# Kernel tuning notes

Measured on AMD Instinct MI355X. Metric: run time of the kernel, lower is better.

Reference implementation:

```python
import jax, jax.numpy as jnp
import numpy as np

B, W, KD, NC, D, NN, NH, AD, HOPS = 512, 4, 64, 32, 256, 16, 8, 32, 4
DH = D // NH
DFF = 4 * D
P = B * W + B
ROLE_WRITER, ROLE_QUERY = 0, 1


def setup_inputs() -> dict:
    key = jax.random.key(0)
    ks = iter(jax.random.split(key, 40))
    f = lambda shape, s=0.02: jax.random.normal(next(ks), shape, dtype=jnp.float32) * s
    inp = {
        'query_keys': jax.random.normal(next(ks), (B, KD), dtype=jnp.float32),
        'writer_keys': jax.random.normal(next(ks), (B, W, KD), dtype=jnp.float32),
        'key_proj_w': f((KD, D)), 'key_proj_b': jnp.zeros((D,), jnp.float32),
        'class_embed': f((NC, D)), 'role_embed': f((3, D)), 'start_node_embed': f((NN, D)),
        'input_ln_g': jnp.ones((D,), jnp.float32), 'input_ln_b': jnp.zeros((D,), jnp.float32),
        'ln1_g': jnp.ones((NN, D), jnp.float32), 'ln1_b': jnp.zeros((NN, D), jnp.float32),
        'wqkv': f((NN, D, 3 * D)), 'bqkv': jnp.zeros((NN, 3 * D), jnp.float32),
        'wo': f((NN, D, D)), 'bo': jnp.zeros((NN, D), jnp.float32),
        'ln2_g': jnp.ones((NN, D), jnp.float32), 'ln2_b': jnp.zeros((NN, D), jnp.float32),
        'w_fc1': f((NN, D, DFF)), 'b_fc1': jnp.zeros((NN, DFF), jnp.float32),
        'w_fc2': f((NN, DFF, D)), 'b_fc2': jnp.zeros((NN, D), jnp.float32),
        'delta_w': jnp.zeros((D, D), jnp.float32), 'delta_b': jnp.zeros((D,), jnp.float32),
        'dir_w': f((D, D)), 'dir_b': jnp.zeros((D,), jnp.float32),
        'mag_w': f((D, 1)), 'mag_b': jnp.full((1,), 2.5, jnp.float32),
        'out_w': f((D, NC)), 'out_b': jnp.zeros((NC,), jnp.float32),
        'address_table': jax.random.normal(next(ks), (NN, AD), dtype=jnp.float32),
        'query_start_nodes': jax.random.randint(next(ks), (B,), 0, NN),
        'writer_labels': jax.random.randint(next(ks), (B, W), 0, NC),
        'writer_start_nodes': jax.random.randint(next(ks), (B, W), 0, NN),
    }
    return inp


def _ln(x):
    m = jnp.mean(x, -1, keepdims=True)
    v = jnp.var(x, -1, keepdims=True)
    return (x - m) * jax.lax.rsqrt(v + 1e-5)


def _forward(query_keys, writer_keys, key_proj_w, key_proj_b, class_embed, role_embed,
             start_node_embed, input_ln_g, input_ln_b, ln1_g, ln1_b, wqkv, bqkv, wo, bo,
             ln2_g, ln2_b, w_fc1, b_fc1, w_fc2, b_fc2, delta_w, delta_b, dir_w, dir_b,
             mag_w, mag_b, out_w, out_b, address_table,
             query_start_nodes, writer_labels, writer_start_nodes):
    # ---- encode writers (encode_writers) ----
    fk = writer_keys.reshape(-1, KD)          # [B*W, KD]
    fl = writer_labels.reshape(-1)            # [B*W]
    fs = writer_start_nodes.reshape(-1)       # [B*W]
    learned_w = fk @ key_proj_w + key_proj_b + class_embed[fl] + start_node_embed[fs] + role_embed[ROLE_WRITER]
    sw = jnp.zeros_like(learned_w).at[:, :KD].set(fk)
    sw = sw.at[:, KD:KD + NC].set(jax.nn.one_hot(fl, NC, dtype=learned_w.dtype))
    enc_w = _ln(learned_w) * input_ln_g + input_ln_b + sw
    # ---- encode queries (encode_queries) ----
    learned_q = query_keys @ key_proj_w + key_proj_b + start_node_embed[query_start_nodes] + role_embed[ROLE_QUERY]
    sq = jnp.zeros_like(learned_q).at[:, :KD].set(query_keys)
    enc_q = _ln(learned_q) * input_ln_g + input_ln_b + sq

    h = jnp.concatenate([enc_w, enc_q], axis=0)          # [P, D]
    node = jnp.concatenate([fs, query_start_nodes], 0)   # [P] current compute node per packet

    inv_sqrt_dh = 1.0 / np.sqrt(DH).astype(np.float32)
    for _ in range(HOPS):
        oh = jax.nn.one_hot(node, NN, dtype=h.dtype)      # [P, NN] dispatch weights

        def pnl(x, Wn, bn):
            # per-node linear: gather-compute-scatter via MoE-style dense dispatch
            xe = jnp.einsum('pn,pd->npd', oh, x)          # [NN, P, din]
            ye = jnp.einsum('npd,ndf->npf', xe, Wn)       # [NN, P, dout]
            return jnp.einsum('npf,pn->pf', ye, oh) + oh @ bn

        # ComputeNodeCell: pre-LN attention among packets at the same node
        x = _ln(h) * (oh @ ln1_g) + oh @ ln1_b
        qkv = pnl(x, wqkv, bqkv)                          # [P, 3D]
        q, k, v = jnp.split(qkv, 3, axis=-1)
        q = q.reshape(P, NH, DH); k = k.reshape(P, NH, DH); v = v.reshape(P, NH, DH)
        scores = jnp.einsum('phd,qhd->hpq', q, k) * inv_sqrt_dh   # [NH, P, P]
        same = node[:, None] == node[None, :]
        scores = jnp.where(same[None], scores, -1e9)
        attn = jax.nn.softmax(scores, axis=-1)
        ao = jnp.einsum('hpq,qhd->phd', attn, v).reshape(P, D)
        h = h + pnl(ao, wo, bo)
        # MLP block
        x2 = _ln(h) * (oh @ ln2_g) + oh @ ln2_b
        h = h + pnl(jax.nn.gelu(pnl(x2, w_fc1, b_fc1)), w_fc2, b_fc2)
        # routing heads: pick next node from address table, apply gated delta
        direction = h @ dir_w + dir_b
        node = jnp.argmax(direction[:, :AD] @ address_table.T, axis=-1)
        h = h + (h @ delta_w + delta_b) * jax.nn.sigmoid(h @ mag_w + mag_b)

    return h @ out_w + out_b                              # [P, NC] per-packet logits


def reference(query_keys, writer_keys, key_proj_w, key_proj_b, class_embed, role_embed,
              start_node_embed, input_ln_g, input_ln_b, ln1_g, ln1_b, wqkv, bqkv, wo, bo,
              ln2_g, ln2_b, w_fc1, b_fc1, w_fc2, b_fc2, delta_w, delta_b, dir_w, dir_b,
              mag_w, mag_b, out_w, out_b, address_table,
              query_start_nodes, writer_labels, writer_start_nodes):
    return _forward(query_keys, writer_keys, key_proj_w, key_proj_b, class_embed, role_embed,
                    start_node_embed, input_ln_g, input_ln_b, ln1_g, ln1_b, wqkv, bqkv, wo, bo,
                    ln2_g, ln2_b, w_fc1, b_fc1, w_fc2, b_fc2, delta_w, delta_b, dir_w, dir_b,
                    mag_w, mag_b, out_w, out_b, address_table,
                    query_start_nodes, writer_labels, writer_start_nodes)
```

## Files before the change

kernel.cpp:

```cpp
#include <hip/hip_runtime.h>
#include <math.h>

#define B_    512
#define W_    4
#define KD_   64
#define NC_   32
#define D_    256
#define NN_   16
#define NH_   8
#define AD_   32
#define HOPS_ 4
#define DH_   32
#define DFF_  1024
#define P_    2560
#define BW_   2048
#define MAXT_ 56

#define INV_SQRT_DH 0.17677669529663687f

__device__ __forceinline__ float block_sum256(float v, float* red) {
#pragma unroll
  for (int off = 32; off > 0; off >>= 1) v += __shfl_xor(v, off, 64);
  int wid = threadIdx.x >> 6;
  if ((threadIdx.x & 63) == 0) red[wid] = v;
  __syncthreads();
  float s = red[0] + red[1] + red[2] + red[3];
  __syncthreads();
  return s;
}

__device__ __forceinline__ float gelu_tanh(float v) {
  float u = 0.7978845608028654f * (v + 0.044715f * v * v * v);
  return 0.5f * v * (1.0f + tanhf(u));
}

__global__ __launch_bounds__(256) void encode_kernel(
    const float* __restrict__ query_keys, const float* __restrict__ writer_keys,
    const float* __restrict__ kpw, const float* __restrict__ kpb,
    const float* __restrict__ ce, const float* __restrict__ re,
    const float* __restrict__ sne, const float* __restrict__ ilg,
    const float* __restrict__ ilb, const int* __restrict__ qsn,
    const int* __restrict__ wl, const int* __restrict__ wsn,
    float* __restrict__ h, int* __restrict__ node) {
  int p = blockIdx.x, t = threadIdx.x;
  __shared__ float fk[KD_];
  __shared__ float red[4];
  const float* key;
  int lab = -1, sn, role;
  if (p < BW_) { key = writer_keys + (size_t)p * KD_; lab = wl[p]; sn = wsn[p]; role = 0; }
  else { int b = p - BW_; key = query_keys + (size_t)b * KD_; sn = qsn[b]; role = 1; }
  if (t < KD_) fk[t] = key[t];
  __syncthreads();

  float acc = kpb[t] + sne[sn * D_ + t] + re[role * D_ + t];
  if (lab >= 0) acc += ce[lab * D_ + t];
#pragma unroll 8
  for (int i = 0; i < KD_; i++) acc += fk[i] * kpw[i * D_ + t];

  float mean = block_sum256(acc, red) * (1.0f / D_);
  float d = acc - mean;
  float var = block_sum256(d * d, red) * (1.0f / D_);
  float xn = d * (1.0f / sqrtf(var + 1e-5f));

  float sw = 0.0f;
  if (t < KD_) sw = fk[t];
  else if (lab >= 0 && t < KD_ + NC_) sw = (t - KD_ == lab) ? 1.0f : 0.0f;

  h[(size_t)p * D_ + t] = xn * ilg[t] + ilb[t] + sw;
  if (t == 0) node[p] = sn;
}

__global__ __launch_bounds__(256) void sort_kernel(const int* __restrict__ node,
                                                   int* __restrict__ order,
                                                   int* __restrict__ offs,
                                                   int* __restrict__ cnts,
                                                   int* __restrict__ tnode,
                                                   int* __restrict__ tstart,
                                                   int* __restrict__ tend,
                                                   int* __restrict__ ntiles) {
  __shared__ int c[NN_], o[NN_], cur[NN_];
  int t = threadIdx.x;
  if (t < NN_) c[t] = 0;
  __syncthreads();
  for (int p = t; p < P_; p += 256) atomicAdd(&c[node[p]], 1);
  __syncthreads();
  if (t == 0) {
    int s = 0;
    for (int n = 0; n < NN_; n++) { o[n] = s; cur[n] = s; s += c[n]; }
    int idx = 0;
    for (int n = 0; n < NN_; n++) {
      int e = o[n] + c[n];
      for (int m0 = o[n]; m0 < e; m0 += 64) {
        tnode[idx] = n; tstart[idx] = m0; tend[idx] = e; idx++;
      }
    }
    ntiles[0] = idx;
  }
  __syncthreads();
  if (t < NN_) { cnts[t] = c[t]; offs[t] = o[t]; }
  for (int p = t; p < P_; p += 256) {
    int r = atomicAdd(&cur[node[p]], 1);
    order[r] = p;
  }
}

__global__ __launch_bounds__(256) void ln_affine(const float* __restrict__ h,
                                                 const float* __restrict__ g,
                                                 const float* __restrict__ b,
                                                 const int* __restrict__ node,
                                                 const int* __restrict__ order,
                                                 float* __restrict__ x) {
  int sp = blockIdx.x, t = threadIdx.x;
  __shared__ float red[4];
  int p = order[sp];
  int n = node[p];
  float v = h[(size_t)p * D_ + t];
  float mean = block_sum256(v, red) * (1.0f / D_);
  float d = v - mean;
  float var = block_sum256(d * d, red) * (1.0f / D_);
  float xn = d * (1.0f / sqrtf(var + 1e-5f));
  x[(size_t)sp * D_ + t] = xn * g[n * D_ + t] + b[n * D_ + t];
}

template <int DIN, int DOUT, int JT, int ACT, int RESID, int PER_NODE, int KSPLIT>
__global__ __launch_bounds__(256) void glin(const float* __restrict__ x,
                                            const float* __restrict__ W,
                                            const float* __restrict__ bias,
                                            float* __restrict__ out,
                                            float* __restrict__ pbuf,
                                            const int* __restrict__ order,
                                            const int* __restrict__ tnode,
                                            const int* __restrict__ tstart,
                                            const int* __restrict__ tend,
                                            const int* __restrict__ ntiles) {
  constexpr int KC = 32, STX = 68;
  constexpr int CPT = JT / 16;
  constexpr int KLEN = DIN / KSPLIT;
  constexpr int NCH = KLEN / KC;
  constexpr int LPR = JT / 4;
  constexpr int RPI = 64 / LPR;

  int ti = blockIdx.x;
  int n, s0, s1;
  if (PER_NODE) {
    if (ti >= ntiles[0]) return;
    n = tnode[ti]; s0 = tstart[ti]; s1 = tend[ti];
  } else {
    n = 0; s0 = ti * 64; s1 = P_;
  }
  int jbase = blockIdx.y * JT;
  int kz = (KSPLIT > 1) ? blockIdx.z : 0;
  int k0 = kz * KLEN;
  int rows = s1 - s0; if (rows > 64) rows = 64;

  __shared__ float xs[2][KC][STX];
  __shared__ float ws[2][KC][JT];

  int tid = threadIdx.x;
  const float* Wn = W + (size_t)n * DIN * DOUT + jbase;

  int xrow = tid >> 2, xq = tid & 3;
  bool xvalid = xrow < rows;
  const float* xptr = x + (size_t)(s0 + (xvalid ? xrow : 0)) * DIN + k0 + xq * 4;

  float4 xr0, xr1;
  auto xfetch = [&](int kc) {
    if (xvalid) {
      xr0 = *(const float4*)(xptr + kc);
      xr1 = *(const float4*)(xptr + kc + 16);
    } else {
      xr0 = make_float4(0.f, 0.f, 0.f, 0.f);
      xr1 = make_float4(0.f, 0.f, 0.f, 0.f);
    }
  };
  auto xstage = [&](int buf) {
    xs[buf][xq * 4 + 0][xrow] = xr0.x;
    xs[buf][xq * 4 + 1][xrow] = xr0.y;
    xs[buf][xq * 4 + 2][xrow] = xr0.z;
    xs[buf][xq * 4 + 3][xrow] = xr0.w;
    xs[buf][xq * 4 + 16][xrow] = xr1.x;
    xs[buf][xq * 4 + 17][xrow] = xr1.y;
    xs[buf][xq * 4 + 18][xrow] = xr1.z;
    xs[buf][xq * 4 + 19][xrow] = xr1.w;
  };
  int wvw = tid >> 6, lane = tid & 63;
  int wlr = lane / LPR;
  int wlc = (lane % LPR) * 4;
  auto wfetch = [&](int buf, int kc) {
#pragma unroll
    for (int i = 0; i < 8 / RPI; i++) {
      int kr = wvw * 8 + i * RPI;
      const float* g = &Wn[(size_t)(k0 + kc + kr + wlr) * DOUT + wlc];
      __builtin_amdgcn_global_load_lds(
          (const __attribute__((address_space(1))) unsigned int*)g,
          (__attribute__((address_space(3))) unsigned int*)&ws[buf][kr][0],
          16, 0, 0);
    }
  };

  wfetch(0, 0);
  xfetch(0);
  xstage(0);
  __syncthreads();

  int r4 = (tid >> 4) * 4;
  int jc = (tid & 15) * CPT;
  float acc[4][CPT];
#pragma unroll
  for (int r = 0; r < 4; r++)
#pragma unroll
    for (int cc = 0; cc < CPT; cc++) acc[r][cc] = 0.f;

  for (int c = 0; c < NCH; c++) {
    int cur = c & 1;
    if (c + 1 < NCH) {
      wfetch(cur ^ 1, (c + 1) * KC);
      xfetch((c + 1) * KC);
    }
#pragma unroll 8
    for (int k = 0; k < KC; k++) {
      float4 a = *(const float4*)&xs[cur][k][r4];
      float av[4] = {a.x, a.y, a.z, a.w};
      float bv[CPT];
      float4 b0 = *(const float4*)&ws[cur][k][jc];
      bv[0] = b0.x; bv[1] = b0.y; bv[2] = b0.z; bv[3] = b0.w;
      if (CPT == 8) {
        float4 b1 = *(const float4*)&ws[cur][k][jc + 4];
        bv[4] = b1.x; bv[5] = b1.y; bv[6] = b1.z; bv[7] = b1.w;
      }
#pragma unroll
      for (int r = 0; r < 4; r++)
#pragma unroll
        for (int cc = 0; cc < CPT; cc++) acc[r][cc] += av[r] * bv[cc];
    }
    if (c + 1 < NCH) xstage(cur ^ 1);
    __syncthreads();
  }

  bool main_part = (KSPLIT == 1) || (kz == 0);
  float bbv[CPT];
#pragma unroll
  for (int cc = 0; cc < CPT; cc++) bbv[cc] = bias[n * DOUT + jbase + jc + cc];

#pragma unroll
  for (int r = 0; r < 4; r++) {
    int lr = r4 + r;
    if (lr >= rows) continue;
    float v[CPT];
    if (main_part) {
#pragma unroll
      for (int cc = 0; cc < CPT; cc++) {
        v[cc] = acc[r][cc] + bbv[cc];
        if (ACT == 1) v[cc] = gelu_tanh(v[cc]);
      }
      if (RESID) {
        int pp = PER_NODE ? order[s0 + lr] : (s0 + lr);
        float* op = &out[(size_t)pp * DOUT + jbase + jc];
#pragma unroll
        for (int cc = 0; cc < CPT; cc += 4) {
          float4 old = *(const float4*)(op + cc);
          *(float4*)(op + cc) =
              make_float4(v[cc] + old.x, v[cc + 1] + old.y, v[cc + 2] + old.z, v[cc + 3] + old.w);
        }
      } else {
        float* op = &out[(size_t)(s0 + lr) * DOUT + jbase + jc];
#pragma unroll
        for (int cc = 0; cc < CPT; cc += 4)
          *(float4*)(op + cc) = make_float4(v[cc], v[cc + 1], v[cc + 2], v[cc + 3]);
      }
    } else {
      float* op = &pbuf[(size_t)(s0 + lr) * DOUT + jbase + jc];
#pragma unroll
      for (int cc = 0; cc < CPT; cc += 4)
        *(float4*)(op + cc) = make_float4(acc[r][cc], acc[r][cc + 1], acc[r][cc + 2], acc[r][cc + 3]);
    }
  }
}

__global__ __launch_bounds__(256) void reduce_kernel(float* __restrict__ h,
                                                     const float* __restrict__ pbuf,
                                                     const int* __restrict__ order) {
  int sp = blockIdx.x, t = threadIdx.x;
  int p = order[sp];
  h[(size_t)p * D_ + t] += pbuf[(size_t)sp * D_ + t];
}

#define ATS 36
__global__ __launch_bounds__(256) void attn_kernel(const float* __restrict__ qkv,
                                                   const int* __restrict__ node,
                                                   const int* __restrict__ order,
                                                   const int* __restrict__ offs,
                                                   const int* __restrict__ cnts,
                                                   float* __restrict__ ao) {
  __shared__ float qs[32 * ATS];
  __shared__ float kts[32 * ATS];
  __shared__ float vs[32 * ATS];
  __shared__ float ps[32 * ATS];
  __shared__ int glo[32], ghi[32];

  int t = threadIdx.x;
  int r = t >> 3;
  int j4 = (t & 7) * 4;
  int r0 = blockIdx.x * 32;
  int hd = blockIdx.y;

  if (t < 32) {
    int n = node[order[r0 + t]];
    glo[t] = offs[n];
    ghi[t] = offs[n] + cnts[n];
  }
  __syncthreads();

  {
    const float* qp = &qkv[(size_t)(r0 + r) * 768 + hd * 32 + j4];
    float4 q4 = *(const float4*)qp;
    q4.x *= INV_SQRT_DH; q4.y *= INV_SQRT_DH; q4.z *= INV_SQRT_DH; q4.w *= INV_SQRT_DH;
    *(float4*)&qs[r * ATS + j4] = q4;
  }

  int lo = glo[0];
  int hi = ghi[31];
  int myglo = glo[r], myghi = ghi[r];

  float4 o4 = {0.f, 0.f, 0.f, 0.f};
  float mrow = -1e30f, lrow = 0.f;

  for (int kt = lo; kt < hi; kt += 32) {
    int sj = kt + r;
    float4 k4 = {0.f, 0.f, 0.f, 0.f}, v4 = {0.f, 0.f, 0.f, 0.f};
    if (sj < hi) {
      const float* kp = &qkv[(size_t)sj * 768 + 256 + hd * 32 + j4];
      k4 = *(const float4*)kp;
      v4 = *(const float4*)(kp + 256);
    }
    __syncthreads();
    kts[(j4 + 0) * ATS + r] = k4.x;
    kts[(j4 + 1) * ATS + r] = k4.y;
    kts[(j4 + 2) * ATS + r] = k4.z;
    kts[(j4 + 3) * ATS + r] = k4.w;
    *(float4*)&vs[r * ATS + j4] = v4;
    __syncthreads();

    float s0 = 0.f, s1 = 0.f, s2 = 0.f, s3 = 0.f;
#pragma unroll 8
    for (int d = 0; d < 32; d++) {
      float qv = qs[r * ATS + d];
      float4 kv = *(const float4*)&kts[d * ATS + j4];
      s0 += qv * kv.x; s1 += qv * kv.y; s2 += qv * kv.z; s3 += qv * kv.w;
    }
    int c0 = kt + j4;
    if (c0 + 0 < myglo || c0 + 0 >= myghi) s0 = -1e30f;
    if (c0 + 1 < myglo || c0 + 1 >= myghi) s1 = -1e30f;
    if (c0 + 2 < myglo || c0 + 2 >= myghi) s2 = -1e30f;
    if (c0 + 3 < myglo || c0 + 3 >= myghi) s3 = -1e30f;

    float mx = fmaxf(fmaxf(s0, s1), fmaxf(s2, s3));
#pragma unroll
    for (int off = 4; off > 0; off >>= 1) mx = fmaxf(mx, __shfl_xor(mx, off, 8));
    float mnew = fmaxf(mrow, mx);
    float alpha = __expf(mrow - mnew);
    float p0 = __expf(s0 - mnew), p1 = __expf(s1 - mnew);
    float p2 = __expf(s2 - mnew), p3 = __expf(s3 - mnew);
    float ls = p0 + p1 + p2 + p3;
#pragma unroll
    for (int off = 4; off > 0; off >>= 1) ls += __shfl_xor(ls, off, 8);
    lrow = lrow * alpha + ls;
    mrow = mnew;
    o4.x *= alpha; o4.y *= alpha; o4.z *= alpha; o4.w *= alpha;

    *(float4*)&ps[r * ATS + j4] = make_float4(p0, p1, p2, p3);
#pragma unroll 8
    for (int j = 0; j < 32; j++) {
      float pj = ps[r * ATS + j];
      float4 vv = *(const float4*)&vs[j * ATS + j4];
      o4.x += pj * vv.x; o4.y += pj * vv.y; o4.z += pj * vv.z; o4.w += pj * vv.w;
    }
  }

  float inv = 1.f / lrow;
  o4.x *= inv; o4.y *= inv; o4.z *= inv; o4.w *= inv;
  *(float4*)&ao[(size_t)(r0 + r) * D_ + hd * 32 + j4] = o4;
}

__global__ __launch_bounds__(256) void route_kernel(float* __restrict__ h,
                                                    const float* __restrict__ dir_w,
                                                    const float* __restrict__ dir_b,
                                                    const float* __restrict__ at,
                                                    const float* __restrict__ mag_w,
                                                    const float* __restrict__ mag_b,
                                                    const float* __restrict__ delta,
                                                    int* __restrict__ node) {
  int p = blockIdx.x, t = threadIdx.x;
  __shared__ float hs[D_];
  __shared__ float dpart[8][AD_];
  __shared__ float dirs[AD_];
  __shared__ float scs[NN_];
  __shared__ float red[4];
  float hv = h[(size_t)p * D_ + t];
  hs[t] = hv;
  __syncthreads();

  int j = t & 31, seg = t >> 5;
  float part = 0.0f;
#pragma unroll 8
  for (int i = 0; i < 32; i++) {
    int ii = seg * 32 + i;
    part += hs[ii] * dir_w[ii * D_ + j];
  }
  dpart[seg][j] = part;
  __syncthreads();
  if (t < AD_) {
    float s = dir_b[t];
#pragma unroll
    for (int g = 0; g < 8; g++) s += dpart[g][t];
    dirs[t] = s;
  }
  __syncthreads();
  if (t < NN_) {
    float s = 0.0f;
#pragma unroll
    for (int a = 0; a < AD_; a++) s += dirs[a] * at[t * AD_ + a];
    scs[t] = s;
  }
  __syncthreads();
  if (t == 0) {
    float best = scs[0];
    int arg = 0;
    for (int nn = 1; nn < NN_; nn++)
      if (scs[nn] > best) { best = scs[nn]; arg = nn; }
    node[p] = arg;
  }
  float mag = block_sum256(hv * mag_w[t], red) + mag_b[0];
  float sig = 1.0f / (1.0f + __expf(-mag));
  h[(size_t)p * D_ + t] = hv + delta[(size_t)p * D_ + t] * sig;
}

__global__ __launch_bounds__(256) void out_kernel(const float* __restrict__ h,
                                                  const float* __restrict__ ow,
                                                  const float* __restrict__ ob,
                                                  float* __restrict__ out) {
  int p = blockIdx.x, t = threadIdx.x;
  __shared__ float hs[D_];
  __shared__ float part[8][NC_];
  hs[t] = h[(size_t)p * D_ + t];
  __syncthreads();
  int j = t & 31, seg = t >> 5;
  float s = 0.0f;
#pragma unroll 8
  for (int i = 0; i < 32; i++) {
    int ii = seg * 32 + i;
    s += hs[ii] * ow[ii * NC_ + j];
  }
  part[seg][j] = s;
  __syncthreads();
  if (t < NC_) {
    float r = ob[t];
#pragma unroll
    for (int g = 0; g < 8; g++) r += part[g][t];
    out[(size_t)p * NC_ + t] = r;
  }
}

extern "C" void kernel_launch(void* const* d_in, const int* in_sizes, int n_in,
                              void* d_out, int out_size, void* d_ws, size_t ws_size,
                              hipStream_t stream) {
  (void)in_sizes; (void)n_in; (void)out_size; (void)ws_size;
  const float* query_keys       = (const float*)d_in[0];
  const float* writer_keys      = (const float*)d_in[1];
  const float* key_proj_w       = (const float*)d_in[2];
  const float* key_proj_b       = (const float*)d_in[3];
  const float* class_embed      = (const float*)d_in[4];
  const float* role_embed       = (const float*)d_in[5];
  const float* start_node_embed = (const float*)d_in[6];
  const float* input_ln_g       = (const float*)d_in[7];
  const float* input_ln_b       = (const float*)d_in[8];
  const float* ln1_g            = (const float*)d_in[9];
  const float* ln1_b            = (const float*)d_in[10];
  const float* wqkv             = (const float*)d_in[11];
  const float* bqkv             = (const float*)d_in[12];
  const float* wo               = (const float*)d_in[13];
  const float* bo               = (const float*)d_in[14];
  const float* ln2_g            = (const float*)d_in[15];
  const float* ln2_b            = (const float*)d_in[16];
  const float* w_fc1            = (const float*)d_in[17];
  const float* b_fc1            = (const float*)d_in[18];
  const float* w_fc2            = (const float*)d_in[19];
  const float* b_fc2            = (const float*)d_in[20];
  const float* delta_w          = (const float*)d_in[21];
  const float* delta_b          = (const float*)d_in[22];
  const float* dir_w            = (const float*)d_in[23];
  const float* dir_b            = (const float*)d_in[24];
  const float* mag_w            = (const float*)d_in[25];
  const float* mag_b            = (const float*)d_in[26];
  const float* out_w            = (const float*)d_in[27];
  const float* out_b            = (const float*)d_in[28];
  const float* address_table    = (const float*)d_in[29];
  const int* query_start_nodes  = (const int*)d_in[30];
  const int* writer_labels      = (const int*)d_in[31];
  const int* writer_start_nodes = (const int*)d_in[32];

  uintptr_t basep = (uintptr_t)d_ws;
  auto carve = [&](size_t bytes) {
    basep = (basep + 255) & ~(uintptr_t)255;
    void* r = (void*)basep;
    basep += bytes;
    return r;
  };
  float* h    = (float*)carve((size_t)P_ * D_ * 4);
  float* x    = (float*)carve((size_t)P_ * D_ * 4);
  float* qkvb = (float*)carve((size_t)P_ * 3 * D_ * 4);
  float* ff   = (float*)carve((size_t)P_ * DFF_ * 4);
  float* pbuf = (float*)carve((size_t)P_ * D_ * 4);
  int* node   = (int*)carve(P_ * 4);
  int* order  = (int*)carve(P_ * 4);
  int* offs   = (int*)carve(NN_ * 4);
  int* cnts   = (int*)carve(NN_ * 4);
  int* tnode  = (int*)carve(MAXT_ * 4);
  int* tstart = (int*)carve(MAXT_ * 4);
  int* tend   = (int*)carve(MAXT_ * 4);
  int* ntiles = (int*)carve(4);

  encode_kernel<<<P_, 256, 0, stream>>>(query_keys, writer_keys, key_proj_w, key_proj_b,
                                        class_embed, role_embed, start_node_embed,
                                        input_ln_g, input_ln_b, query_start_nodes,
                                        writer_labels, writer_start_nodes, h, node);

  for (int hop = 0; hop < HOPS_; ++hop) {
    sort_kernel<<<1, 256, 0, stream>>>(node, order, offs, cnts,
                                       tnode, tstart, tend, ntiles);
    ln_affine<<<P_, 256, 0, stream>>>(h, ln1_g, ln1_b, node, order, x);
    glin<256, 768, 128, 0, 0, 1, 1><<<dim3(MAXT_, 6), 256, 0, stream>>>(
        x, wqkv, bqkv, qkvb, nullptr, order, tnode, tstart, tend, ntiles);
    attn_kernel<<<dim3(P_ / 32, NH_), 256, 0, stream>>>(qkvb, node, order, offs, cnts,
                                                        x );
    glin<256, 256, 64, 0, 1, 1, 1><<<dim3(MAXT_, 4), 256, 0, stream>>>(
        x, wo, bo, h, nullptr, order, tnode, tstart, tend, ntiles);
    ln_affine<<<P_, 256, 0, stream>>>(h, ln2_g, ln2_b, node, order, x);
    glin<256, 1024, 128, 1, 0, 1, 1><<<dim3(MAXT_, 8), 256, 0, stream>>>(
        x, w_fc1, b_fc1, ff, nullptr, order, tnode, tstart, tend, ntiles);
    glin<1024, 256, 128, 0, 1, 1, 2><<<dim3(MAXT_, 2, 2), 256, 0, stream>>>(
        ff, w_fc2, b_fc2, h, pbuf, order, tnode, tstart, tend, ntiles);
    reduce_kernel<<<P_, 256, 0, stream>>>(h, pbuf, order);
    glin<256, 256, 64, 0, 0, 0, 1><<<dim3(P_ / 64, 4), 256, 0, stream>>>(
        h, delta_w, delta_b, qkvb , nullptr, order,
        tnode, tstart, tend, ntiles);
    route_kernel<<<P_, 256, 0, stream>>>(h, dir_w, dir_b, address_table, mag_w, mag_b,
                                         qkvb, node);
  }

  out_kernel<<<P_, 256, 0, stream>>>(h, out_w, out_b, (float*)d_out);
}
```

Measured before the change: 1.001 ms.

## Fuse split-K partial reduction into delta linear and route kernels via inverse order

Removes the separate reduce_kernel that added the second split-K partial of the fc2 GEMM into h. The delta linear now adds the pbuf partial while loading its input, and route_kernel adds it when reading h. Both look up the partial's row through a new inverse permutation built in sort_kernel. Separately, the glin thread-to-column mapping is changed so each thread's two float4 column groups sit HALF=64 columns apart instead of being adjacent, which changes the LDS read and global store access pattern.

```diff
diff --git a/kernel.cpp b/kernel.cpp
--- a/kernel.cpp
+++ b/kernel.cpp
@@ -72,6 +72,7 @@
 
 __global__ __launch_bounds__(256) void sort_kernel(const int* __restrict__ node,
                                                    int* __restrict__ order,
+                                                   int* __restrict__ invord,
                                                    int* __restrict__ offs,
                                                    int* __restrict__ cnts,
                                                    int* __restrict__ tnode,
@@ -101,6 +102,7 @@
   for (int p = t; p < P_; p += 256) {
     int r = atomicAdd(&cur[node[p]], 1);
     order[r] = p;
+    invord[p] = r;
   }
 }
 
@@ -122,19 +124,21 @@
   x[(size_t)sp * D_ + t] = xn * g[n * D_ + t] + b[n * D_ + t];
 }
 
-template <int DIN, int DOUT, int JT, int ACT, int RESID, int PER_NODE, int KSPLIT>
+template <int DIN, int DOUT, int JT, int ACT, int RESID, int PER_NODE, int KSPLIT, int ADDP>
 __global__ __launch_bounds__(256) void glin(const float* __restrict__ x,
                                             const float* __restrict__ W,
                                             const float* __restrict__ bias,
                                             float* __restrict__ out,
                                             float* __restrict__ pbuf,
                                             const int* __restrict__ order,
+                                            const int* __restrict__ invord,
                                             const int* __restrict__ tnode,
                                             const int* __restrict__ tstart,
                                             const int* __restrict__ tend,
                                             const int* __restrict__ ntiles) {
   constexpr int KC = 32, STX = 68;
   constexpr int CPT = JT / 16;
+  constexpr int HALF = 64;
   constexpr int KLEN = DIN / KSPLIT;
   constexpr int NCH = KLEN / KC;
   constexpr int LPR = JT / 4;
@@ -162,12 +166,23 @@
   int xrow = tid >> 2, xq = tid & 3;
   bool xvalid = xrow < rows;
   const float* xptr = x + (size_t)(s0 + (xvalid ? xrow : 0)) * DIN + k0 + xq * 4;
+  const float* pptr = nullptr;
+  if (ADDP) {
+    int pr = xvalid ? invord[s0 + xrow] : 0;
+    pptr = pbuf + (size_t)pr * DIN + k0 + xq * 4;
+  }
 
   float4 xr0, xr1;
   auto xfetch = [&](int kc) {
     if (xvalid) {
       xr0 = *(const float4*)(xptr + kc);
       xr1 = *(const float4*)(xptr + kc + 16);
+      if (ADDP) {
+        float4 p0 = *(const float4*)(pptr + kc);
+        float4 p1 = *(const float4*)(pptr + kc + 16);
+        xr0.x += p0.x; xr0.y += p0.y; xr0.z += p0.z; xr0.w += p0.w;
+        xr1.x += p1.x; xr1.y += p1.y; xr1.z += p1.z; xr1.w += p1.w;
+      }
     } else {
       xr0 = make_float4(0.f, 0.f, 0.f, 0.f);
       xr1 = make_float4(0.f, 0.f, 0.f, 0.f);
@@ -204,7 +219,7 @@
   __syncthreads();
 
   int r4 = (tid >> 4) * 4;
-  int jc = (tid & 15) * CPT;
+  int jc4 = (tid & 15) * 4;
   float acc[4][CPT];
 #pragma unroll
   for (int r = 0; r < 4; r++)
@@ -222,10 +237,10 @@
       float4 a = *(const float4*)&xs[cur][k][r4];
       float av[4] = {a.x, a.y, a.z, a.w};
       float bv[CPT];
-      float4 b0 = *(const float4*)&ws[cur][k][jc];
+      float4 b0 = *(const float4*)&ws[cur][k][jc4];
       bv[0] = b0.x; bv[1] = b0.y; bv[2] = b0.z; bv[3] = b0.w;
       if (CPT == 8) {
-        float4 b1 = *(const float4*)&ws[cur][k][jc + 4];
+        float4 b1 = *(const float4*)&ws[cur][k][jc4 + HALF];
         bv[4] = b1.x; bv[5] = b1.y; bv[6] = b1.z; bv[7] = b1.w;
       }
 #pragma unroll
@@ -240,7 +255,11 @@
   bool main_part = (KSPLIT == 1) || (kz == 0);
   float bbv[CPT];
 #pragma unroll
-  for (int cc = 0; cc < CPT; cc++) bbv[cc] = bias[n * DOUT + jbase + jc + cc];
+  for (int cc = 0; cc < 4; cc++) bbv[cc] = bias[n * DOUT + jbase + jc4 + cc];
+  if (CPT == 8) {
+#pragma unroll
+    for (int cc = 0; cc < 4; cc++) bbv[4 + cc] = bias[n * DOUT + jbase + jc4 + HALF + cc];
+  }
 
 #pragma unroll
   for (int r = 0; r < 4; r++) {
@@ -255,34 +274,29 @@
       }
       if (RESID) {
         int pp = PER_NODE ? order[s0 + lr] : (s0 + lr);
-        float* op = &out[(size_t)pp * DOUT + jbase + jc];
-#pragma unroll
-        for (int cc = 0; cc < CPT; cc += 4) {
-          float4 old = *(const float4*)(op + cc);
-          *(float4*)(op + cc) =
-              make_float4(v[cc] + old.x, v[cc + 1] + old.y, v[cc + 2] + old.z, v[cc + 3] + old.w);
+        float* op = &out[(size_t)pp * DOUT + jbase + jc4];
+        {
+          float4 old = *(const float4*)op;
+          *(float4*)op = make_float4(v[0] + old.x, v[1] + old.y, v[2] + old.z, v[3] + old.w);
+        }
+        if (CPT == 8) {
+          float4 old = *(const float4*)(op + HALF);
+          *(float4*)(op + HALF) =
+              make_float4(v[4] + old.x, v[5] + old.y, v[6] + old.z, v[7] + old.w);
         }
       } else {
-        float* op = &out[(size_t)(s0 + lr) * DOUT + jbase + jc];
-#pragma unroll
-        for (int cc = 0; cc < CPT; cc += 4)
-          *(float4*)(op + cc) = make_float4(v[cc], v[cc + 1], v[cc + 2], v[cc + 3]);
+        float* op = &out[(size_t)(s0 + lr) * DOUT + jbase + jc4];
+        *(float4*)op = make_float4(v[0], v[1], v[2], v[3]);
+        if (CPT == 8)
+          *(float4*)(op + HALF) = make_float4(v[4], v[5], v[6], v[7]);
       }
     } else {
-      float* op = &pbuf[(size_t)(s0 + lr) * DOUT + jbase + jc];
-#pragma unroll
-      for (int cc = 0; cc < CPT; cc += 4)
-        *(float4*)(op + cc) = make_float4(acc[r][cc], acc[r][cc + 1], acc[r][cc + 2], acc[r][cc + 3]);
-    }
-  }
-}
-
-__global__ __launch_bounds__(256) void reduce_kernel(float* __restrict__ h,
-                                                     const float* __restrict__ pbuf,
-                                                     const int* __restrict__ order) {
-  int sp = blockIdx.x, t = threadIdx.x;
-  int p = order[sp];
-  h[(size_t)p * D_ + t] += pbuf[(size_t)sp * D_ + t];
+      float* op = &pbuf[(size_t)(s0 + lr) * DOUT + jbase + jc4];
+      *(float4*)op = make_float4(acc[r][0], acc[r][1], acc[r][2], acc[r][3]);
+      if (CPT == 8)
+        *(float4*)(op + HALF) = make_float4(acc[r][4], acc[r][5], acc[r][6], acc[r][7]);
+    }
+  }
 }
 
 #define ATS 36
@@ -383,6 +397,8 @@
 }
 
 __global__ __launch_bounds__(256) void route_kernel(float* __restrict__ h,
+                                                    const float* __restrict__ pbuf,
+                                                    const int* __restrict__ invord,
                                                     const float* __restrict__ dir_w,
                                                     const float* __restrict__ dir_b,
                                                     const float* __restrict__ at,
@@ -396,7 +412,7 @@
   __shared__ float dirs[AD_];
   __shared__ float scs[NN_];
   __shared__ float red[4];
-  float hv = h[(size_t)p * D_ + t];
+  float hv = h[(size_t)p * D_ + t] + pbuf[(size_t)invord[p] * D_ + t];
   hs[t] = hv;
   __syncthreads();
 
@@ -513,6 +529,7 @@
   float* pbuf = (float*)carve((size_t)P_ * D_ * 4);
   int* node   = (int*)carve(P_ * 4);
   int* order  = (int*)carve(P_ * 4);
+  int* invord = (int*)carve(P_ * 4);
   int* offs   = (int*)carve(NN_ * 4);
   int* cnts   = (int*)carve(NN_ * 4);
   int* tnode  = (int*)carve(MAXT_ * 4);
@@ -526,26 +543,25 @@
                                         writer_labels, writer_start_nodes, h, node);
 
   for (int hop = 0; hop < HOPS_; ++hop) {
-    sort_kernel<<<1, 256, 0, stream>>>(node, order, offs, cnts,
+    sort_kernel<<<1, 256, 0, stream>>>(node, order, invord, offs, cnts,
                                        tnode, tstart, tend, ntiles);
     ln_affine<<<P_, 256, 0, stream>>>(h, ln1_g, ln1_b, node, order, x);
-    glin<256, 768, 128, 0, 0, 1, 1><<<dim3(MAXT_, 6), 256, 0, stream>>>(
-        x, wqkv, bqkv, qkvb, nullptr, order, tnode, tstart, tend, ntiles);
+    glin<256, 768, 128, 0, 0, 1, 1, 0><<<dim3(MAXT_, 6), 256, 0, stream>>>(
+        x, wqkv, bqkv, qkvb, nullptr, order, invord, tnode, tstart, tend, ntiles);
     attn_kernel<<<dim3(P_ / 32, NH_), 256, 0, stream>>>(qkvb, node, order, offs, cnts,
                                                         x );
-    glin<256, 256, 64, 0, 1, 1, 1><<<dim3(MAXT_, 4), 256, 0, stream>>>(
-        x, wo, bo, h, nullptr, order, tnode, tstart, tend, ntiles);
+    glin<256, 256, 64, 0, 1, 1, 1, 0><<<dim3(MAXT_, 4), 256, 0, stream>>>(
+        x, wo, bo, h, nullptr, order, invord, tnode, tstart, tend, ntiles);
     ln_affine<<<P_, 256, 0, stream>>>(h, ln2_g, ln2_b, node, order, x);
-    glin<256, 1024, 128, 1, 0, 1, 1><<<dim3(MAXT_, 8), 256, 0, stream>>>(
-        x, w_fc1, b_fc1, ff, nullptr, order, tnode, tstart, tend, ntiles);
-    glin<1024, 256, 128, 0, 1, 1, 2><<<dim3(MAXT_, 2, 2), 256, 0, stream>>>(
-        ff, w_fc2, b_fc2, h, pbuf, order, tnode, tstart, tend, ntiles);
-    reduce_kernel<<<P_, 256, 0, stream>>>(h, pbuf, order);
-    glin<256, 256, 64, 0, 0, 0, 1><<<dim3(P_ / 64, 4), 256, 0, stream>>>(
-        h, delta_w, delta_b, qkvb , nullptr, order,
+    glin<256, 1024, 128, 1, 0, 1, 1, 0><<<dim3(MAXT_, 8), 256, 0, stream>>>(
+        x, w_fc1, b_fc1, ff, nullptr, order, invord, tnode, tstart, tend, ntiles);
+    glin<1024, 256, 128, 0, 1, 1, 2, 0><<<dim3(MAXT_, 2, 2), 256, 0, stream>>>(
+        ff, w_fc2, b_fc2, h, pbuf, order, invord, tnode, tstart, tend, ntiles);
+    glin<256, 256, 64, 0, 0, 0, 1, 1><<<dim3(P_ / 64, 4), 256, 0, stream>>>(
+        h, delta_w, delta_b, qkvb , pbuf, order, invord,
         tnode, tstart, tend, ntiles);
-    route_kernel<<<P_, 256, 0, stream>>>(h, dir_w, dir_b, address_table, mag_w, mag_b,
-                                         qkvb, node);
+    route_kernel<<<P_, 256, 0, stream>>>(h, pbuf, invord, dir_w, dir_b, address_table,
+                                         mag_w, mag_b, qkvb, node);
   }
 
   out_kernel<<<P_, 256, 0, stream>>>(h, out_w, out_b, (float*)d_out);
```

New measurement: 962.8 us. 3.8% less time.
